# Kernel optimization log

Hardware: AMD Instinct MI355X
Metric: run time of the kernel (lower is better)

## Reference

```python
import jax, jax.numpy as jnp
import numpy as np

B, L, M = 4, 2048, 1024
G, E = 8, 8
CAP_FACTOR = 2.0

def _ffn_size(m, widening=8.0):
    f = int(widening * m) * 2 // 3
    return f + (8 - f) % 8

H = _ffn_size(M)  # 5464


def setup_inputs():
    key = jax.random.key(0)
    k0, k1, k2, k3, k4 = jax.random.split(key, 5)
    return {
        "inputs": jax.random.normal(k0, (B, L, M), jnp.float32),
        "router_w": jax.random.normal(k1, (M, E), jnp.float32) * 0.02,
        "w0_kernel": jax.random.normal(k2, (E, M, H), jnp.float32) * 0.02,
        "w1_kernel": jax.random.normal(k3, (E, M, H), jnp.float32) * 0.02,
        "wo_kernel": jax.random.normal(k4, (E, H, M), jnp.float32) * 0.02,
    }


def _gating_top2(logits, C):
    # logits: (G, S, E) -> dispatch, combine: (G, S, E, C)
    Gd, Sd, Ed = logits.shape
    raw = jax.nn.softmax(logits, axis=-1)
    idx1 = jnp.argmax(raw, axis=-1)
    m1 = jax.nn.one_hot(idx1, Ed, dtype=logits.dtype)
    gate1 = jnp.sum(raw * m1, axis=-1)
    rest = raw * (1.0 - m1)
    idx2 = jnp.argmax(rest, axis=-1)
    m2 = jax.nn.one_hot(idx2, Ed, dtype=logits.dtype)
    gate2 = jnp.sum(rest * m2, axis=-1)
    # exclusive cumsum along S gives position in expert queue
    p1 = jnp.cumsum(m1, axis=-2) - m1
    m1 = m1 * (p1 < C).astype(m1.dtype)
    p1 = jnp.sum(p1 * m1, axis=-1)
    m1_flat = jnp.sum(m1, axis=-1)
    m1_count = jnp.sum(m1, axis=-2)  # (G, E)
    p2 = jnp.cumsum(m2, axis=-2) - m2 + m1_count[:, None, :]
    m2 = m2 * (p2 < C).astype(m2.dtype)
    p2 = jnp.sum(p2 * m2, axis=-1)
    m2_flat = jnp.sum(m2, axis=-1)
    gate1 = gate1 * m1_flat
    gate2 = gate2 * m2_flat
    c1 = (gate1[..., None] * jax.nn.one_hot(idx1, Ed, dtype=jnp.float32))[..., None] \
         * jax.nn.one_hot(p1.astype(jnp.int32), C, dtype=jnp.float32)[:, :, None, :]
    c2 = (gate2[..., None] * jax.nn.one_hot(idx2, Ed, dtype=jnp.float32))[..., None] \
         * jax.nn.one_hot(p2.astype(jnp.int32), C, dtype=jnp.float32)[:, :, None, :]
    combine = (c1 + c2).astype(logits.dtype)
    dispatch = (combine != 0).astype(logits.dtype)
    return dispatch, combine


def reference(inputs, router_w, w0_kernel, w1_kernel, wo_kernel):
    Bb, Ll, Mm = inputs.shape
    S = Bb * Ll // G
    x = inputs.reshape(G, S, Mm)
    logits = jnp.einsum('GSM,ME->GSE', x, router_w)
    cap = int(CAP_FACTOR * S / E)
    C = (cap + 3) // 4 * 4
    dispatch, combine = _gating_top2(logits, C)
    expert_inputs = jnp.einsum('GSEC,GSM->EGCM', dispatch, x)
    layer_w0 = jnp.einsum('EGCM,EMH->EGCH', expert_inputs, w0_kernel)
    layer_w1 = jnp.einsum('EGCM,EMH->EGCH', expert_inputs, w1_kernel)
    hidden = jax.nn.gelu(layer_w0, approximate=True) * layer_w1
    expert_outputs = jnp.einsum('EGCH,EHM->EGCM', hidden, wo_kernel)
    out = jnp.einsum('EGCM,GSEC->GSM', expert_outputs, combine)
    return out.reshape(Bb, Ll, Mm)
```

## Files before the change

### kernel.cpp

```cpp
#include <hip/hip_runtime.h>
#include <cstdint>
#include <cstddef>

constexpr int G = 8;
constexpr int S = 1024;
constexpr int E = 8;
constexpr int MD = 1024;
constexpr int H = 5464;
constexpr int HP = 5504;
constexpr int N1 = 2 * HP;
constexpr int CAP = 256;
constexpr int T = G * S;
constexpr int GC = G * CAP;
constexpr int BK = 64;

typedef __bf16 bf16;
typedef __bf16 bf16x8 __attribute__((ext_vector_type(8)));
typedef __bf16 bf16x4 __attribute__((ext_vector_type(4)));
typedef float f32x4 __attribute__((ext_vector_type(4)));

__device__ __forceinline__ void async16(const void* g, void* l) {
    __builtin_amdgcn_global_load_lds((__attribute__((address_space(1))) void*)(g),
                                     (__attribute__((address_space(3))) void*)(l),
                                     16, 0, 0);
}

__device__ __forceinline__ float gelu_tanh(float x) {
    return 0.5f * x * (1.0f + tanhf(0.7978845608028654f * (x + 0.044715f * x * x * x)));
}

__device__ __forceinline__ int sw_elem(int row, int gi) {
    return (row * 8 + (gi ^ (row & 7))) * 8;
}

#define BARRIER()   __builtin_amdgcn_s_barrier()
#define FENCE()     asm volatile("" ::: "memory")
#define WAITV(n)    asm volatile("s_waitcnt vmcnt(" #n ")" ::: "memory")
#define WAITLGKM0() asm volatile("s_waitcnt lgkmcnt(0)" ::: "memory")

__global__ void router_k(const float* __restrict__ x, const float* __restrict__ rw,
                         int* __restrict__ idx1, int* __restrict__ idx2,
                         float* __restrict__ gate1, float* __restrict__ gate2) {
    int wave = threadIdx.x >> 6, lane = threadIdx.x & 63;
    int t = blockIdx.x * 4 + wave;
    const float* xr = x + (size_t)t * MD;
    float acc[E];
#pragma unroll
    for (int e = 0; e < E; e++) acc[e] = 0.0f;
    for (int m = lane; m < MD; m += 64) {
        float xv = xr[m];
        const float* w = rw + m * E;
#pragma unroll
        for (int e = 0; e < E; e++) acc[e] += xv * w[e];
    }
#pragma unroll
    for (int off = 32; off > 0; off >>= 1) {
#pragma unroll
        for (int e = 0; e < E; e++) acc[e] += __shfl_xor(acc[e], off, 64);
    }
    if (lane == 0) {
        float mx = acc[0];
#pragma unroll
        for (int e = 1; e < E; e++) mx = fmaxf(mx, acc[e]);
        float raw[E]; float sum = 0.0f;
#pragma unroll
        for (int e = 0; e < E; e++) { raw[e] = expf(acc[e] - mx); sum += raw[e]; }
        float inv = 1.0f / sum;
#pragma unroll
        for (int e = 0; e < E; e++) raw[e] *= inv;
        int i1 = 0; float b1 = raw[0];
#pragma unroll
        for (int e = 1; e < E; e++) if (raw[e] > b1) { b1 = raw[e]; i1 = e; }
        int i2 = 0; float b2 = -1.0f;
#pragma unroll
        for (int e = 0; e < E; e++) {
            float v = (e == i1) ? 0.0f : raw[e];
            if (v > b2) { b2 = v; i2 = e; }
        }
        idx1[t] = i1; idx2[t] = i2; gate1[t] = b1; gate2[t] = b2;
    }
}

__global__ void scan_k(const int* __restrict__ idx1, const int* __restrict__ idx2,
                       const float* __restrict__ gate1, const float* __restrict__ gate2,
                       int* __restrict__ tok1, int* __restrict__ tok2,
                       float* __restrict__ g1m, float* __restrict__ g2m,
                       int* __restrict__ slot_src, int* __restrict__ fill) {
    int g = blockIdx.x;
    int lane = threadIdx.x;
    unsigned long long lt = (1ull << lane) - 1ull;
    int cnt1[E], cnt2[E];
#pragma unroll
    for (int e = 0; e < E; e++) { cnt1[e] = 0; cnt2[e] = 0; }
    for (int ch = 0; ch < S / 64; ch++) {
        int s = ch * 64 + lane, t = g * S + s;
        int i1 = idx1[t];
        int p = 0;
#pragma unroll
        for (int e = 0; e < E; e++) {
            unsigned long long m = __ballot(i1 == e);
            if (i1 == e) p = cnt1[e] + (int)__popcll(m & lt);
            cnt1[e] += (int)__popcll(m);
        }
        bool kept = p < CAP;
        tok1[t] = kept ? (i1 * CAP + p) : -1;
        g1m[t] = kept ? gate1[t] : 0.0f;
        if (kept) slot_src[((i1 * G + g) << 8) + p] = s;
    }
    int m1c[E];
#pragma unroll
    for (int e = 0; e < E; e++) m1c[e] = min(cnt1[e], CAP);
    for (int ch = 0; ch < S / 64; ch++) {
        int s = ch * 64 + lane, t = g * S + s;
        int i2 = idx2[t];
        float g2 = gate2[t];
        int p = 0;
#pragma unroll
        for (int e = 0; e < E; e++) {
            unsigned long long m = __ballot(i2 == e);
            if (i2 == e) p = m1c[e] + cnt2[e] + (int)__popcll(m & lt);
            cnt2[e] += (int)__popcll(m);
        }
        bool kept = p < CAP;
        bool nz = (g2 != 0.0f);
        tok2[t] = (kept && nz) ? (i2 * CAP + p) : -1;
        g2m[t] = (kept && nz) ? g2 : 0.0f;
        if (kept) slot_src[((i2 * G + g) << 8) + p] = nz ? s : -1;
    }
    if (lane < E) fill[lane * G + g] = min(m1c[lane] + cnt2[lane], CAP);
}

__global__ void gather_k(const float* __restrict__ x, const int* __restrict__ slot_src,
                         const int* __restrict__ fill, bf16* __restrict__ ein) {
    int slot = blockIdx.x;
    int c = slot & 255, g = (slot >> 8) & 7, e = slot >> 11;
    int i = threadIdx.x * 4;
    int src = (c < fill[e * G + g]) ? slot_src[slot] : -1;
    bf16x4 v;
    if (src >= 0) {
        float4 f = *(const float4*)(x + ((size_t)(g * S + src)) * MD + i);
        v[0] = (bf16)f.x; v[1] = (bf16)f.y; v[2] = (bf16)f.z; v[3] = (bf16)f.w;
    } else {
        v[0] = (bf16)0.0f; v[1] = (bf16)0.0f; v[2] = (bf16)0.0f; v[3] = (bf16)0.0f;
    }
    *(bf16x4*)(ein + (size_t)slot * MD + i) = v;
}

__global__ void transpose_cast_k(const float* __restrict__ in, bf16* __restrict__ out,
                                 int R, int Cc, int Rp, int Cp, int ilv) {
    __shared__ float lds[64][65];
    int c0 = blockIdx.x * 64;
    int r0 = blockIdx.y * 64;
    const float* bin = in + (size_t)blockIdx.z * R * Cc;
    bf16* bout = out + (size_t)blockIdx.z * Cp * Rp;
    int tid = threadIdx.x;
    int lr = tid >> 4;
    int lc = (tid & 15) * 4;
#pragma unroll
    for (int i = 0; i < 4; i++) {
        int r = r0 + lr + i * 16;
        float v0 = 0, v1 = 0, v2 = 0, v3 = 0;
        if (r < R) {
            const float* p = bin + (size_t)r * Cc + c0 + lc;
            if (c0 + lc + 3 < Cc) {
                float4 f = *(const float4*)p;
                v0 = f.x; v1 = f.y; v2 = f.z; v3 = f.w;
            } else {
                if (c0 + lc + 0 < Cc) v0 = p[0];
                if (c0 + lc + 1 < Cc) v1 = p[1];
                if (c0 + lc + 2 < Cc) v2 = p[2];
                if (c0 + lc + 3 < Cc) v3 = p[3];
            }
        }
        lds[lr + i * 16][lc + 0] = v0;
        lds[lr + i * 16][lc + 1] = v1;
        lds[lr + i * 16][lc + 2] = v2;
        lds[lr + i * 16][lc + 3] = v3;
    }
    __syncthreads();
    int orr = tid >> 2;
    int oc = (tid & 3) * 16;
    bf16x8 o0, o1;
#pragma unroll
    for (int j = 0; j < 8; j++) o0[j] = (bf16)lds[oc + j][orr];
#pragma unroll
    for (int j = 0; j < 8; j++) o1[j] = (bf16)lds[oc + 8 + j][orr];
    int cc = c0 + orr;
    int r01 = (ilv >= 0) ? (((cc >> 7) << 8) + ilv + (cc & 127)) : cc;
    bf16* dst = bout + (size_t)r01 * Rp + r0 + oc;
    *(bf16x8*)(dst) = o0;
    *(bf16x8*)(dst + 8) = o1;
}

__device__ __forceinline__ void stage_half(const bf16* __restrict__ base, int ld,
                                           bf16* lds, int half, int wave, int lr, int ls) {
#pragma unroll
    for (int i = 0; i < 2; i++) {
        int c = half * 16 + wave * 2 + i;
        int r = c * 8 + lr;
        int gj = ls ^ (r & 7);
        async16(base + (size_t)r * ld + gj * 8, lds + c * 512);
    }
    FENCE();
}

template<int NT>
__device__ __forceinline__ void mm256_core(const bf16* __restrict__ A,
                                           const bf16* __restrict__ B,
                                           int lda, int ldb,
                                           bf16* sA0, bf16* sA1, bf16* sB0, bf16* sB1,
                                           f32x4 (&acc)[8][4]) {
    int lane = threadIdx.x & 63, wave = threadIdx.x >> 6;
    int wm = wave >> 2, wn = wave & 3;
    int lr = lane >> 3, ls = lane & 7;
    int mr = lane & 15, kq = lane >> 4;

    stage_half(A, lda, sA0, 0, wave, lr, ls);
    stage_half(B, ldb, sB0, 0, wave, lr, ls);
    stage_half(A, lda, sA0, 1, wave, lr, ls);
    stage_half(B, ldb, sB0, 1, wave, lr, ls);

    f32x4 z = {0.0f, 0.0f, 0.0f, 0.0f};
#pragma unroll
    for (int i = 0; i < 8; i++)
#pragma unroll
        for (int j = 0; j < 4; j++) acc[i][j] = z;

    WAITV(4);
    BARRIER();

#pragma unroll 1
    for (int t = 0; t < NT; ++t) {
        bf16* Ad = (t & 1) ? sA1 : sA0;
        bf16* Bd = (t & 1) ? sB1 : sB0;
        bf16* An = (t & 1) ? sA0 : sA1;
        bf16* Bn = (t & 1) ? sB0 : sB1;
        const bf16* Ax = A + (size_t)(t + 1) * BK;
        const bf16* Bx = B + (size_t)(t + 1) * BK;
        bool pf = (t + 1 < NT);
        bf16x8 a0[4][2], a1[4][2], b0[2][2], b1[2][2];

#pragma unroll
        for (int i = 0; i < 4; i++)
#pragma unroll
            for (int ks = 0; ks < 2; ks++)
                a0[i][ks] = *(const bf16x8*)&Ad[sw_elem(wm * 64 + i * 16 + mr, ks * 4 + kq)];
#pragma unroll
        for (int j = 0; j < 2; j++)
#pragma unroll
            for (int ks = 0; ks < 2; ks++)
                b0[j][ks] = *(const bf16x8*)&Bd[sw_elem(wn * 32 + j * 16 + mr, ks * 4 + kq)];
        if (pf) { stage_half(Ax, lda, An, 0, wave, lr, ls); WAITV(2); }
        else    { WAITV(0); }
        BARRIER();
        WAITLGKM0();
        __builtin_amdgcn_s_setprio(1);
#pragma unroll
        for (int ks = 0; ks < 2; ks++)
#pragma unroll
            for (int i = 0; i < 4; i++)
#pragma unroll
                for (int j = 0; j < 2; j++)
                    acc[i][j] = __builtin_amdgcn_mfma_f32_16x16x32_bf16(a0[i][ks], b0[j][ks], acc[i][j], 0, 0, 0);
        __builtin_amdgcn_s_setprio(0);
        BARRIER();

#pragma unroll
        for (int j = 0; j < 2; j++)
#pragma unroll
            for (int ks = 0; ks < 2; ks++)
                b1[j][ks] = *(const bf16x8*)&Bd[sw_elem(128 + wn * 32 + j * 16 + mr, ks * 4 + kq)];
        if (pf) stage_half(Bx, ldb, Bn, 0, wave, lr, ls);
        BARRIER();
        WAITLGKM0();
        __builtin_amdgcn_s_setprio(1);
#pragma unroll
        for (int ks = 0; ks < 2; ks++)
#pragma unroll
            for (int i = 0; i < 4; i++)
#pragma unroll
                for (int j = 0; j < 2; j++)
                    acc[i][2 + j] = __builtin_amdgcn_mfma_f32_16x16x32_bf16(a0[i][ks], b1[j][ks], acc[i][2 + j], 0, 0, 0);
        __builtin_amdgcn_s_setprio(0);
        BARRIER();

#pragma unroll
        for (int i = 0; i < 4; i++)
#pragma unroll
            for (int ks = 0; ks < 2; ks++)
                a1[i][ks] = *(const bf16x8*)&Ad[sw_elem(128 + wm * 64 + i * 16 + mr, ks * 4 + kq)];
        if (pf) stage_half(Ax, lda, An, 1, wave, lr, ls);
        BARRIER();
        WAITLGKM0();
        __builtin_amdgcn_s_setprio(1);
#pragma unroll
        for (int ks = 0; ks < 2; ks++)
#pragma unroll
            for (int i = 0; i < 4; i++)
#pragma unroll
                for (int j = 0; j < 2; j++)
                    acc[4 + i][2 + j] = __builtin_amdgcn_mfma_f32_16x16x32_bf16(a1[i][ks], b1[j][ks], acc[4 + i][2 + j], 0, 0, 0);
        __builtin_amdgcn_s_setprio(0);
        BARRIER();

        if (pf) { stage_half(Bx, ldb, Bn, 1, wave, lr, ls); WAITV(4); }
        else    { WAITV(0); }
        BARRIER();
        __builtin_amdgcn_s_setprio(1);
#pragma unroll
        for (int ks = 0; ks < 2; ks++)
#pragma unroll
            for (int i = 0; i < 4; i++)
#pragma unroll
                for (int j = 0; j < 2; j++)
                    acc[4 + i][j] = __builtin_amdgcn_mfma_f32_16x16x32_bf16(a1[i][ks], b0[j][ks], acc[4 + i][j], 0, 0, 0);
        __builtin_amdgcn_s_setprio(0);
        BARRIER();
    }
}

__global__ __launch_bounds__(512, 2) void gemm1_k(const bf16* __restrict__ ein,
                                                  const bf16* __restrict__ w01t,
                                                  bf16* __restrict__ hidden) {
    __shared__ __align__(16) bf16 smem[4 * 256 * BK];
    int flat = blockIdx.x;
    int chunk = gridDim.x >> 3;
    int swz = (flat & 7) * chunk + (flat >> 3);
    constexpr int NTL = N1 / 256;
    int e = swz / (8 * NTL);
    int rem = swz - e * (8 * NTL);
    int rt = rem & 7;
    int nt = rem >> 3;
    const bf16* A = ein  + ((size_t)e * GC + (size_t)rt * 256) * MD;
    const bf16* B = w01t + ((size_t)e * N1 + (size_t)nt * 256) * MD;
    f32x4 acc[8][4];
    mm256_core<MD / BK>(A, B, MD, MD, smem, smem + 16384, smem + 32768, smem + 49152, acc);

    int lane = threadIdx.x & 63, wave = threadIdx.x >> 6;
    int wm = wave >> 2, wn = wave & 3;
    bf16* Hb = hidden + (size_t)e * GC * HP;
#pragma unroll
    for (int i = 0; i < 8; i++) {
        int rowb = rt * 256 + (i >> 2) * 128 + wm * 64 + (i & 3) * 16 + (lane >> 4) * 4;
#pragma unroll
        for (int j = 0; j < 2; j++) {
            int col = nt * 128 + wn * 32 + j * 16 + (lane & 15);
            bool ok = col < H;
#pragma unroll
            for (int r = 0; r < 4; r++) {
                float v = ok ? gelu_tanh(acc[i][j][r]) * acc[i][j + 2][r] : 0.0f;
                Hb[(size_t)(rowb + r) * HP + col] = (bf16)v;
            }
        }
    }
}

__global__ __launch_bounds__(512, 2) void gemm2_k(const bf16* __restrict__ hidden,
                                                  const bf16* __restrict__ wot,
                                                  float* __restrict__ eout) {
    __shared__ __align__(16) bf16 smem[4 * 256 * BK];
    int flat = blockIdx.x;
    int chunk = gridDim.x >> 3;
    int swz = (flat & 7) * chunk + (flat >> 3);
    int e = swz >> 5;
    int rem = swz & 31;
    int rt = rem & 7;
    int nt = rem >> 3;
    const bf16* A = hidden + ((size_t)e * GC + (size_t)rt * 256) * HP;
    const bf16* B = wot    + ((size_t)e * MD + (size_t)nt * 256) * HP;
    f32x4 acc[8][4];
    mm256_core<HP / BK>(A, B, HP, HP, smem, smem + 16384, smem + 32768, smem + 49152, acc);

    int lane = threadIdx.x & 63, wave = threadIdx.x >> 6;
    int wm = wave >> 2, wn = wave & 3;
    float* Ob = eout + (size_t)e * GC * MD;
#pragma unroll
    for (int i = 0; i < 8; i++) {
        int rowb = rt * 256 + (i >> 2) * 128 + wm * 64 + (i & 3) * 16 + (lane >> 4) * 4;
#pragma unroll
        for (int j = 0; j < 4; j++) {
            int col = nt * 256 + (j >> 1) * 128 + wn * 32 + (j & 1) * 16 + (lane & 15);
#pragma unroll
            for (int r = 0; r < 4; r++)
                Ob[(size_t)(rowb + r) * MD + col] = acc[i][j][r];
        }
    }
}

__global__ void combine_k(const float* __restrict__ eout, const int* __restrict__ tok1,
                          const int* __restrict__ tok2, const float* __restrict__ g1m,
                          const float* __restrict__ g2m, float* __restrict__ out) {
    int t = blockIdx.x;
    int g = t >> 10;
    int i = threadIdx.x * 4;
    int r1 = tok1[t], r2 = tok2[t];
    float f1 = g1m[t], f2 = g2m[t];
    float4 o = {0, 0, 0, 0};
    if (r1 >= 0) {
        size_t row = (size_t)(((r1 >> 8) * G + g) * CAP + (r1 & 255));
        float4 v = *(const float4*)(eout + row * MD + i);
        o.x += f1 * v.x; o.y += f1 * v.y; o.z += f1 * v.z; o.w += f1 * v.w;
    }
    if (r2 >= 0) {
        size_t row = (size_t)(((r2 >> 8) * G + g) * CAP + (r2 & 255));
        float4 v = *(const float4*)(eout + row * MD + i);
        o.x += f2 * v.x; o.y += f2 * v.y; o.z += f2 * v.z; o.w += f2 * v.w;
    }
    *(float4*)(out + (size_t)t * MD + i) = o;
}

constexpr size_t SZ_TI = (size_t)T * 4;
constexpr size_t OFF_IDX1 = 0;
constexpr size_t OFF_IDX2 = OFF_IDX1 + SZ_TI;
constexpr size_t OFF_GT1  = OFF_IDX2 + SZ_TI;
constexpr size_t OFF_GT2  = OFF_GT1 + SZ_TI;
constexpr size_t OFF_G1M  = OFF_GT2 + SZ_TI;
constexpr size_t OFF_G2M  = OFF_G1M + SZ_TI;
constexpr size_t OFF_TK1  = OFF_G2M + SZ_TI;
constexpr size_t OFF_TK2  = OFF_TK1 + SZ_TI;
constexpr size_t OFF_SLOT = OFF_TK2 + SZ_TI;
constexpr size_t OFF_FILL = OFF_SLOT + (size_t)E * G * CAP * 4;
constexpr size_t OFF_EIN  = (OFF_FILL + (size_t)E * G * 4 + 255) & ~(size_t)255;
constexpr size_t OFF_W01T = OFF_EIN + (size_t)E * GC * MD * 2;
constexpr size_t OFF_WOT  = OFF_W01T + (size_t)E * N1 * MD * 2;
constexpr size_t OFF_HID  = OFF_WOT + (size_t)E * MD * HP * 2;
constexpr size_t OFF_EOUT = OFF_HID + (size_t)E * GC * HP * 2;

extern "C" void kernel_launch(void* const* d_in, const int* in_sizes, int n_in,
                              void* d_out, int out_size, void* d_ws, size_t ws_size,
                              hipStream_t stream) {
    const float* x  = (const float*)d_in[0];
    const float* rw = (const float*)d_in[1];
    const float* w0 = (const float*)d_in[2];
    const float* w1 = (const float*)d_in[3];
    const float* wo = (const float*)d_in[4];
    float* out = (float*)d_out;
    char* ws = (char*)d_ws;

    int*   idx1 = (int*)(ws + OFF_IDX1);
    int*   idx2 = (int*)(ws + OFF_IDX2);
    float* gt1  = (float*)(ws + OFF_GT1);
    float* gt2  = (float*)(ws + OFF_GT2);
    float* g1m  = (float*)(ws + OFF_G1M);
    float* g2m  = (float*)(ws + OFF_G2M);
    int*   tk1  = (int*)(ws + OFF_TK1);
    int*   tk2  = (int*)(ws + OFF_TK2);
    int*   slot = (int*)(ws + OFF_SLOT);
    int*   fill = (int*)(ws + OFF_FILL);
    bf16*  ein  = (bf16*)(ws + OFF_EIN);
    bf16*  w01t = (bf16*)(ws + OFF_W01T);
    bf16*  wot  = (bf16*)(ws + OFF_WOT);
    bf16*  hid  = (bf16*)(ws + OFF_HID);
    float* eout = (float*)(ws + OFF_EOUT);

    router_k<<<T / 4, 256, 0, stream>>>(x, rw, idx1, idx2, gt1, gt2);
    scan_k<<<G, 64, 0, stream>>>(idx1, idx2, gt1, gt2, tk1, tk2, g1m, g2m, slot, fill);
    gather_k<<<E * G * CAP, 256, 0, stream>>>(x, slot, fill, ein);
    transpose_cast_k<<<dim3(HP / 64, MD / 64, E), 256, 0, stream>>>(w0, w01t, MD, H, MD, N1, 0);
    transpose_cast_k<<<dim3(HP / 64, MD / 64, E), 256, 0, stream>>>(w1, w01t, MD, H, MD, N1, 128);
    transpose_cast_k<<<dim3(MD / 64, HP / 64, E), 256, 0, stream>>>(wo, wot, H, MD, HP, MD, -1);
    gemm1_k<<<dim3((GC / 256) * (N1 / 256) * E), 512, 0, stream>>>(ein, w01t, hid);
    gemm2_k<<<dim3((GC / 256) * (MD / 256) * E), 512, 0, stream>>>(hid, wot, eout);
    combine_k<<<T, 256, 0, stream>>>(eout, tk1, tk2, g1m, g2m, out);
}
```

Measured before the change: 1.208 ms.

## Replace pipelined 256x256 gemm1 with simple 128x64 dual-B tile kernel and fast GELU

Drops the interleaved w0/w1 transposed layout and the shared double-buffered 256x256 MFMA core for gemm1. The new kernel uses a 128-row by 64-column tile that loads separate w0 and w1 tiles and accumulates both in one pass, with 256 threads and single-buffered LDS. GELU now uses an exp plus reciprocal formulation in place of tanhf. The aim is higher occupancy and a cheaper epilogue, at the cost of losing the software pipelining, raising global traffic per FLOP, and synchronising twice per K step.

```diff
diff --git a/kernel.cpp b/kernel.cpp
--- a/kernel.cpp
+++ b/kernel.cpp
@@ -8,7 +8,6 @@
 constexpr int MD = 1024;
 constexpr int H = 5464;
 constexpr int HP = 5504;
-constexpr int N1 = 2 * HP;
 constexpr int CAP = 256;
 constexpr int T = G * S;
 constexpr int GC = G * CAP;
@@ -25,8 +24,11 @@
                                      16, 0, 0);
 }
 
-__device__ __forceinline__ float gelu_tanh(float x) {
-    return 0.5f * x * (1.0f + tanhf(0.7978845608028654f * (x + 0.044715f * x * x * x)));
+__device__ __forceinline__ float gelu_fast(float x) {
+    float u = 0.7978845608028654f * (x + 0.044715f * x * x * x);
+    float t = __expf(-2.0f * fabsf(u));
+    float th = (1.0f - t) * __builtin_amdgcn_rcpf(1.0f + t);
+    return 0.5f * x * (1.0f + copysignf(th, u));
 }
 
 __device__ __forceinline__ int sw_elem(int row, int gi) {
@@ -147,7 +149,7 @@
 }
 
 __global__ void transpose_cast_k(const float* __restrict__ in, bf16* __restrict__ out,
-                                 int R, int Cc, int Rp, int Cp, int ilv) {
+                                 int R, int Cc, int Rp, int Cp) {
     __shared__ float lds[64][65];
     int c0 = blockIdx.x * 64;
     int r0 = blockIdx.y * 64;
@@ -185,11 +187,96 @@
     for (int j = 0; j < 8; j++) o0[j] = (bf16)lds[oc + j][orr];
 #pragma unroll
     for (int j = 0; j < 8; j++) o1[j] = (bf16)lds[oc + 8 + j][orr];
-    int cc = c0 + orr;
-    int r01 = (ilv >= 0) ? (((cc >> 7) << 8) + ilv + (cc & 127)) : cc;
-    bf16* dst = bout + (size_t)r01 * Rp + r0 + oc;
+    bf16* dst = bout + (size_t)(c0 + orr) * Rp + r0 + oc;
     *(bf16x8*)(dst) = o0;
     *(bf16x8*)(dst + 8) = o1;
+}
+
+__global__ __launch_bounds__(256, 3) void gemm1_k(const bf16* __restrict__ ein,
+                                                  const bf16* __restrict__ w0t,
+                                                  const bf16* __restrict__ w1t,
+                                                  bf16* __restrict__ hidden) {
+    __shared__ __align__(16) bf16 As[128 * 64];
+    __shared__ __align__(16) bf16 B0s[64 * 64];
+    __shared__ __align__(16) bf16 B1s[64 * 64];
+    int flat = blockIdx.x;
+    int chunk = gridDim.x >> 3;
+    int swz = (flat & 7) * chunk + (flat >> 3);
+    int e = swz / 1376;
+    int rem = swz - e * 1376;
+    int rt = rem & 15;
+    int nt = rem >> 4;
+    int lane = threadIdx.x & 63, wave = threadIdx.x >> 6;
+    int wm = wave & 1, wn = wave >> 1;
+    const bf16* A  = ein + ((size_t)e * GC + rt * 128) * MD;
+    const bf16* B0 = w0t + ((size_t)e * HP + nt * 64) * MD;
+    const bf16* B1 = w1t + ((size_t)e * HP + nt * 64) * MD;
+    f32x4 acc0[4][2], acc1[4][2];
+    f32x4 z = {0.0f, 0.0f, 0.0f, 0.0f};
+#pragma unroll
+    for (int i = 0; i < 4; i++)
+#pragma unroll
+        for (int j = 0; j < 2; j++) { acc0[i][j] = z; acc1[i][j] = z; }
+    int lr = lane >> 3, ls = lane & 7;
+#pragma unroll 1
+    for (int kt = 0; kt < MD / 64; kt++) {
+        __syncthreads();
+        int k0 = kt * 64;
+#pragma unroll
+        for (int i = 0; i < 4; i++) {
+            int c = i * 4 + wave;
+            int r = c * 8 + lr;
+            int gj = ls ^ (r & 7);
+            async16(A + (size_t)r * MD + k0 + gj * 8, &As[c * 512]);
+        }
+#pragma unroll
+        for (int i = 0; i < 2; i++) {
+            int c = i * 4 + wave;
+            int r = c * 8 + lr;
+            int gj = ls ^ (r & 7);
+            size_t go = (size_t)r * MD + k0 + gj * 8;
+            async16(B0 + go, &B0s[c * 512]);
+            async16(B1 + go, &B1s[c * 512]);
+        }
+        __syncthreads();
+#pragma unroll
+        for (int ks = 0; ks < 2; ks++) {
+            bf16x8 af[4], b0f[2], b1f[2];
+            int gi = ks * 4 + (lane >> 4);
+            int mrow = wm * 64 + (lane & 15);
+            int nrow = wn * 32 + (lane & 15);
+#pragma unroll
+            for (int i = 0; i < 4; i++) af[i] = *(const bf16x8*)&As[sw_elem(mrow + i * 16, gi)];
+#pragma unroll
+            for (int j = 0; j < 2; j++) {
+                b0f[j] = *(const bf16x8*)&B0s[sw_elem(nrow + j * 16, gi)];
+                b1f[j] = *(const bf16x8*)&B1s[sw_elem(nrow + j * 16, gi)];
+            }
+#pragma unroll
+            for (int i = 0; i < 4; i++)
+#pragma unroll
+                for (int j = 0; j < 2; j++) {
+                    acc0[i][j] = __builtin_amdgcn_mfma_f32_16x16x32_bf16(af[i], b0f[j], acc0[i][j], 0, 0, 0);
+                    acc1[i][j] = __builtin_amdgcn_mfma_f32_16x16x32_bf16(af[i], b1f[j], acc1[i][j], 0, 0, 0);
+                }
+        }
+    }
+    bf16* Hb = hidden + (size_t)e * GC * HP;
+    int colb = nt * 64 + wn * 32 + (lane & 15);
+    int rowb = rt * 128 + wm * 64 + ((lane >> 4) * 4);
+#pragma unroll
+    for (int i = 0; i < 4; i++)
+#pragma unroll
+        for (int j = 0; j < 2; j++) {
+            int col = colb + j * 16;
+            bool ok = col < H;
+#pragma unroll
+            for (int r = 0; r < 4; r++) {
+                int row = rowb + i * 16 + r;
+                float v = ok ? gelu_fast(acc0[i][j][r]) * acc1[i][j][r] : 0.0f;
+                Hb[(size_t)row * HP + col] = (bf16)v;
+            }
+        }
 }
 
 __device__ __forceinline__ void stage_half(const bf16* __restrict__ base, int ld,
@@ -316,42 +403,6 @@
                     acc[4 + i][j] = __builtin_amdgcn_mfma_f32_16x16x32_bf16(a1[i][ks], b0[j][ks], acc[4 + i][j], 0, 0, 0);
         __builtin_amdgcn_s_setprio(0);
         BARRIER();
-    }
-}
-
-__global__ __launch_bounds__(512, 2) void gemm1_k(const bf16* __restrict__ ein,
-                                                  const bf16* __restrict__ w01t,
-                                                  bf16* __restrict__ hidden) {
-    __shared__ __align__(16) bf16 smem[4 * 256 * BK];
-    int flat = blockIdx.x;
-    int chunk = gridDim.x >> 3;
-    int swz = (flat & 7) * chunk + (flat >> 3);
-    constexpr int NTL = N1 / 256;
-    int e = swz / (8 * NTL);
-    int rem = swz - e * (8 * NTL);
-    int rt = rem & 7;
-    int nt = rem >> 3;
-    const bf16* A = ein  + ((size_t)e * GC + (size_t)rt * 256) * MD;
-    const bf16* B = w01t + ((size_t)e * N1 + (size_t)nt * 256) * MD;
-    f32x4 acc[8][4];
-    mm256_core<MD / BK>(A, B, MD, MD, smem, smem + 16384, smem + 32768, smem + 49152, acc);
-
-    int lane = threadIdx.x & 63, wave = threadIdx.x >> 6;
-    int wm = wave >> 2, wn = wave & 3;
-    bf16* Hb = hidden + (size_t)e * GC * HP;
-#pragma unroll
-    for (int i = 0; i < 8; i++) {
-        int rowb = rt * 256 + (i >> 2) * 128 + wm * 64 + (i & 3) * 16 + (lane >> 4) * 4;
-#pragma unroll
-        for (int j = 0; j < 2; j++) {
-            int col = nt * 128 + wn * 32 + j * 16 + (lane & 15);
-            bool ok = col < H;
-#pragma unroll
-            for (int r = 0; r < 4; r++) {
-                float v = ok ? gelu_tanh(acc[i][j][r]) * acc[i][j + 2][r] : 0.0f;
-                Hb[(size_t)(rowb + r) * HP + col] = (bf16)v;
-            }
-        }
     }
 }
 
@@ -421,8 +472,9 @@
 constexpr size_t OFF_SLOT = OFF_TK2 + SZ_TI;
 constexpr size_t OFF_FILL = OFF_SLOT + (size_t)E * G * CAP * 4;
 constexpr size_t OFF_EIN  = (OFF_FILL + (size_t)E * G * 4 + 255) & ~(size_t)255;
-constexpr size_t OFF_W01T = OFF_EIN + (size_t)E * GC * MD * 2;
-constexpr size_t OFF_WOT  = OFF_W01T + (size_t)E * N1 * MD * 2;
+constexpr size_t OFF_W0T  = OFF_EIN + (size_t)E * GC * MD * 2;
+constexpr size_t OFF_W1T  = OFF_W0T + (size_t)E * HP * MD * 2;
+constexpr size_t OFF_WOT  = OFF_W1T + (size_t)E * HP * MD * 2;
 constexpr size_t OFF_HID  = OFF_WOT + (size_t)E * MD * HP * 2;
 constexpr size_t OFF_EOUT = OFF_HID + (size_t)E * GC * HP * 2;
 
@@ -448,7 +500,8 @@
     int*   slot = (int*)(ws + OFF_SLOT);
     int*   fill = (int*)(ws + OFF_FILL);
     bf16*  ein  = (bf16*)(ws + OFF_EIN);
-    bf16*  w01t = (bf16*)(ws + OFF_W01T);
+    bf16*  w0t  = (bf16*)(ws + OFF_W0T);
+    bf16*  w1t  = (bf16*)(ws + OFF_W1T);
     bf16*  wot  = (bf16*)(ws + OFF_WOT);
     bf16*  hid  = (bf16*)(ws + OFF_HID);
     float* eout = (float*)(ws + OFF_EOUT);
@@ -456,10 +509,10 @@
     router_k<<<T / 4, 256, 0, stream>>>(x, rw, idx1, idx2, gt1, gt2);
     scan_k<<<G, 64, 0, stream>>>(idx1, idx2, gt1, gt2, tk1, tk2, g1m, g2m, slot, fill);
     gather_k<<<E * G * CAP, 256, 0, stream>>>(x, slot, fill, ein);
-    transpose_cast_k<<<dim3(HP / 64, MD / 64, E), 256, 0, stream>>>(w0, w01t, MD, H, MD, N1, 0);
-    transpose_cast_k<<<dim3(HP / 64, MD / 64, E), 256, 0, stream>>>(w1, w01t, MD, H, MD, N1, 128);
-    transpose_cast_k<<<dim3(MD / 64, HP / 64, E), 256, 0, stream>>>(wo, wot, H, MD, HP, MD, -1);
-    gemm1_k<<<dim3((GC / 256) * (N1 / 256) * E), 512, 0, stream>>>(ein, w01t, hid);
+    transpose_cast_k<<<dim3(HP / 64, MD / 64, E), 256, 0, stream>>>(w0, w0t, MD, H, MD, HP);
+    transpose_cast_k<<<dim3(HP / 64, MD / 64, E), 256, 0, stream>>>(w1, w1t, MD, H, MD, HP);
+    transpose_cast_k<<<dim3(MD / 64, HP / 64, E), 256, 0, stream>>>(wo, wot, H, MD, HP, MD);
+    gemm1_k<<<dim3(16 * 86 * 8), 256, 0, stream>>>(ein, w0t, w1t, hid);
     gemm2_k<<<dim3((GC / 256) * (MD / 256) * E), 512, 0, stream>>>(hid, wot, eout);
     combine_k<<<T, 256, 0, stream>>>(eout, tk1, tk2, g1m, g2m, out);
 }
```

Result: faster. 1.122 ms (-7.1%).
